# Kernel tuning notes

Measured on AMD Instinct MI355X. Metric: run time of the kernel, lower is better.

## Reference

```python
import jax, jax.numpy as jnp
import numpy as np

SIZES = [4096, 12288, 20480, 20480, 8192]  # atoms of degree 0..4 (atoms sorted by degree)
N_ATOMS = sum(SIZES)
BATCH = 1024
N_TASKS, N_CLASSES = 12, 2
BN_EPS = 1e-3  # keras BatchNormalization default epsilon


def setup_inputs() -> dict:
    key = jax.random.key(0)
    ks = jax.random.split(key, 20)
    inp = {}
    inp["atom_features"] = jax.random.normal(ks[0], (N_ATOMS, 75), jnp.float32)
    starts = np.concatenate([[0], np.cumsum(SIZES)[:-1]])
    inp["degree_slice"] = jnp.asarray(np.stack([starts, np.array(SIZES)], 1), jnp.int32)
    inp["membership"] = jax.random.randint(ks[1], (N_ATOMS,), 0, BATCH, jnp.int32)
    inp["n_samples"] = BATCH
    for d in range(1, 5):
        inp[f"deg_adj_{d}"] = jax.random.randint(ks[1 + d], (SIZES[d], d), 0, N_ATOMS, jnp.int32)

    def w(k, shape, s=0.05):
        return s * jax.random.normal(k, shape, jnp.float32)

    # GraphConv weights: order [relW_deg1, selfW_deg1, ..., relW_deg4, selfW_deg4, selfW_deg0]
    inp["gc1_W"] = w(ks[6], (9, 75, 256)); inp["gc1_b"] = w(ks[7], (9, 256))
    inp["gc2_W"] = w(ks[8], (9, 256, 256)); inp["gc2_b"] = w(ks[9], (9, 256))

    def bn_params(k, c):  # rows: gamma, beta, moving_mean, moving_var
        g = 1.0 + 0.1 * jax.random.normal(k, (c,), jnp.float32)
        b = 0.1 * jax.random.normal(jax.random.fold_in(k, 1), (c,), jnp.float32)
        return jnp.stack([g, b, jnp.zeros((c,), jnp.float32), jnp.ones((c,), jnp.float32)])

    inp["bn1"] = bn_params(ks[10], 256)
    inp["bn2"] = bn_params(ks[11], 256)
    inp["bn3"] = bn_params(ks[12], 512)
    inp["dense_W"] = w(ks[13], (256, 512)); inp["dense_b"] = w(ks[14], (512,))
    inp["head_W"] = w(ks[15], (2 * 512, N_TASKS * N_CLASSES)); inp["head_b"] = w(ks[16], (N_TASKS * N_CLASSES,))
    return inp


def _graph_conv(x, adjs, W, b):
    # degree-0 atoms: self transform only (last weight matrix)
    pieces = [x[: SIZES[0]] @ W[8] + b[8]]
    off = SIZES[0]
    for d in range(1, 5):
        nd = SIZES[d]
        self_atoms = x[off: off + nd]
        rel = jnp.take(x, adjs[d - 1], axis=0).sum(axis=1)  # [nd, F] neighbor sum
        out = rel @ W[2 * (d - 1)] + b[2 * (d - 1)] + self_atoms @ W[2 * d - 1] + b[2 * d - 1]
        pieces.append(out)
        off += nd
    return jax.nn.relu(jnp.concatenate(pieces, axis=0))


def _graph_pool(x, adjs):
    pieces = [x[: SIZES[0]]]  # degree-0: passthrough
    off = SIZES[0]
    for d in range(1, 5):
        nd = SIZES[d]
        self_atoms = x[off: off + nd]
        neigh = jnp.take(x, adjs[d - 1], axis=0)  # [nd, d, F]
        pieces.append(jnp.maximum(self_atoms, neigh.max(axis=1)))
        off += nd
    return jnp.concatenate(pieces, axis=0)


def _bn(x, p):  # inference batchnorm with moving stats
    g, b, m, v = p
    return g * (x - m) * jax.lax.rsqrt(v + BN_EPS) + b


def reference(atom_features, degree_slice, membership, n_samples,
              deg_adj_1, deg_adj_2, deg_adj_3, deg_adj_4,
              gc1_W, gc1_b, gc2_W, gc2_b, bn1, bn2, bn3,
              dense_W, dense_b, head_W, head_b):
    adjs = (deg_adj_1, deg_adj_2, deg_adj_3, deg_adj_4)
    x = atom_features
    for W, b, bn in ((gc1_W, gc1_b, bn1), (gc2_W, gc2_b, bn2)):
        x = _bn(_graph_conv(x, adjs, W, b), bn)
        x = _graph_pool(x, adjs)
    h = _bn(jax.nn.relu(x @ dense_W + dense_b), bn3)  # [N_ATOMS, 512]
    # GraphGather: per-molecule sum and max, tanh activation
    seg_sum = jax.ops.segment_sum(h, membership, num_segments=BATCH)
    seg_max = jax.ops.segment_max(h, membership, num_segments=BATCH)
    fp = jnp.tanh(jnp.concatenate([seg_sum, seg_max], axis=1))  # neural fingerprint [BATCH, 1024]
    logits = (fp @ head_W + head_b).reshape(BATCH, N_TASKS, N_CLASSES)[: int(n_samples)]  # trim
    return jax.nn.softmax(logits, axis=-1), logits, fp
```

## Files before the change

### kernel.cpp

```cpp
#include <hip/hip_runtime.h>
#include <hip/hip_bf16.h>
#include <math.h>

#define NA 65536
#define MAXSEG 160

typedef _Float16 half8 __attribute__((ext_vector_type(8)));
typedef _Float16 h4    __attribute__((ext_vector_type(4)));
typedef float float4v  __attribute__((ext_vector_type(4)));

typedef __attribute__((address_space(3))) unsigned int lds_uint;
typedef __attribute__((address_space(1))) const unsigned int g_uint;

__device__ __forceinline__ void async16(const void* g, void* l) {
    __builtin_amdgcn_global_load_lds((g_uint*)g, (lds_uint*)l, 16, 0, 0);
}


__device__ __forceinline__ int unperm128(int p) {
    return (p & ~127) + (((p & 127) & 7) << 4) + ((p & 127) >> 3);
}

__device__ __forceinline__ void atom_seg(int atom, int& d, int& loc,
                                         const int* a1, const int* a2,
                                         const int* a3, const int* a4,
                                         const int*& adj) {
    if (atom < 4096)       { d = 0; loc = 0; adj = nullptr; }
    else if (atom < 16384) { d = 1; adj = a1; loc = atom - 4096; }
    else if (atom < 36864) { d = 2; adj = a2; loc = atom - 16384; }
    else if (atom < 57344) { d = 3; adj = a3; loc = atom - 36864; }
    else                   { d = 4; adj = a4; loc = atom - 57344; }
}

__global__ __launch_bounds__(256) void prep_kernel(
    const float* __restrict__ af,
    const float* __restrict__ gc1W, const float* __restrict__ gc1b,
    const float* __restrict__ gc2W, const float* __restrict__ gc2b,
    const float* __restrict__ dW, const float* __restrict__ hW,
    _Float16* __restrict__ af16, _Float16* __restrict__ Wc1, float* __restrict__ bias1,
    _Float16* __restrict__ Wc2, float* __restrict__ bias2,
    _Float16* __restrict__ dWt, float* __restrict__ hWt, int* __restrict__ count) {
    int b = blockIdx.x, t = threadIdx.x;
    if (b < 5120) {
        int idx = b * 256 + t;
        int atom = idx / 20, k4 = idx - atom * 20;
        int c0 = k4 * 4;
        h4 o;
        #pragma unroll
        for (int j = 0; j < 4; j++) {
            int c = c0 + j;
            o[j] = (_Float16)((c < 75) ? af[(size_t)atom * 75 + c] : 0.f);
        }
        *(h4*)(af16 + (size_t)atom * 80 + c0) = o;
    } else if (b < 5920) {
        int idx = (b - 5120) * 256 + t;
        if (idx < 204800) {
            int k = idx % 160, n = (idx / 160) & 255, seg = idx / (160 * 256);
            float v = 0.f;
            if (k < 80) {
                if (k < 75) { int w = (seg == 0) ? 8 : (2 * seg - 1); v = gc1W[(w * 75 + k) * 256 + n]; }
            } else {
                int kk = k - 80;
                if (kk < 75 && seg > 0) { int w = 2 * (seg - 1); v = gc1W[(w * 75 + kk) * 256 + n]; }
            }
            Wc1[(size_t)(seg * 256 + n) * 160 + k] = (_Float16)v;
        }
        if (idx < 1280) {
            int n = idx & 255, seg = idx >> 8;
            bias1[idx] = (seg == 0) ? gc1b[8 * 256 + n]
                                    : gc1b[(2 * seg - 1) * 256 + n] + gc1b[2 * (seg - 1) * 256 + n];
        }
    } else if (b < 8480) {
        int idx = (b - 5920) * 256 + t;
        int k = idx & 511, n = (idx >> 9) & 255, seg = idx >> 17;
        float v = 0.f;
        if (k < 256) {
            int w = (seg == 0) ? 8 : (2 * seg - 1);
            v = gc2W[(w * 256 + unperm128(k)) * 256 + n];
        } else if (seg > 0) {
            int w = 2 * (seg - 1);
            v = gc2W[(w * 256 + unperm128(k - 256)) * 256 + n];
        }
        Wc2[(size_t)(seg * 256 + n) * 512 + k] = (_Float16)v;
        if (idx < 1280) {
            int nn = idx & 255, sg = idx >> 8;
            bias2[idx] = (sg == 0) ? gc2b[8 * 256 + nn]
                                   : gc2b[(2 * sg - 1) * 256 + nn] + gc2b[2 * (sg - 1) * 256 + nn];
        }
    } else if (b < 8992) {
        int idx = (b - 8480) * 256 + t;
        int n = idx >> 8, k = idx & 255;
        dWt[(size_t)n * 256 + k] = (_Float16)dW[(size_t)unperm128(k) * 512 + n];
    } else if (b < 9088) {
        int idx = (b - 8992) * 256 + t;
        int o = idx / 1024, k = idx & 1023;
        hWt[idx] = hW[k * 24 + o];
    } else {
        int i = (b - 9088) * 256 + t;
        if (i < 1024) count[i] = 0;
    }
}

__global__ void bucket_kernel(const int* __restrict__ mem, int* __restrict__ count,
                              int* __restrict__ list) {
    int i = blockIdx.x * 256 + threadIdx.x;
    int seg = mem[i];
    int pos = atomicAdd(&count[seg], 1);
    if (pos < MAXSEG) list[seg * MAXSEG + pos] = i;
}

__global__ __launch_bounds__(256) void gather1n_kernel(
    const _Float16* __restrict__ af16,
    const int* __restrict__ a1, const int* __restrict__ a2,
    const int* __restrict__ a3, const int* __restrict__ a4,
    _Float16* __restrict__ Xn1) {
    int idx = blockIdx.x * 256 + threadIdx.x;
    int atom = idx / 20, k4 = idx - atom * 20;
    int c0 = k4 * 4;
    int d, loc; const int* adj;
    atom_seg(atom, d, loc, a1, a2, a3, a4, adj);
    float s0 = 0.f, s1 = 0.f, s2 = 0.f, s3 = 0.f;
    for (int j = 0; j < d; j++) {
        int nb = adj[(size_t)loc * d + j];
        h4 v = *(const h4*)(af16 + (size_t)nb * 80 + c0);
        s0 += (float)v[0]; s1 += (float)v[1]; s2 += (float)v[2]; s3 += (float)v[3];
    }
    h4 o; o[0] = (_Float16)s0; o[1] = (_Float16)s1; o[2] = (_Float16)s2; o[3] = (_Float16)s3;
    *(h4*)(Xn1 + (size_t)atom * 80 + c0) = o;
}

__global__ __launch_bounds__(256) void gather2n_kernel(
    const _Float16* __restrict__ p,
    const int* __restrict__ a1, const int* __restrict__ a2,
    const int* __restrict__ a3, const int* __restrict__ a4,
    _Float16* __restrict__ Xn) {
    int atom = blockIdx.x * 8 + (threadIdx.x >> 5);
    int l = threadIdx.x & 31;
    int d, loc; const int* adj;
    atom_seg(atom, d, loc, a1, a2, a3, a4, adj);
    float s[8] = {};
    for (int j = 0; j < d; j++) {
        int nb = adj[(size_t)loc * d + j];
        half8 v = *(const half8*)(p + (size_t)nb * 256 + l * 8);
        #pragma unroll
        for (int e = 0; e < 8; e++) s[e] += (float)v[e];
    }
    half8 o;
    #pragma unroll
    for (int e = 0; e < 8; e++) o[e] = (_Float16)s[e];
    *(half8*)(Xn + (size_t)atom * 256 + l * 8) = o;
}

template<int K, int N, int BK, int SB>
__global__ __launch_bounds__(256) void gemm_kernel(
    const _Float16* __restrict__ X, const _Float16* __restrict__ Xn,
    const _Float16* __restrict__ Wt,
    const float* __restrict__ bias, const float* __restrict__ bnp,
    int wstride, int bstride, _Float16* __restrict__ out) {
    constexpr int NC8 = BK / 8;
    constexpr int MASK = NC8 - 1;
    __shared__ __align__(16) _Float16 As[128 * BK];
    __shared__ __align__(16) _Float16 Bs[128 * BK];
    constexpr int nb = N / 128;
    int G = gridDim.x;
    int bid = (blockIdx.x & 7) * (G >> 3) + (blockIdx.x >> 3);
    int m0 = (bid / nb) * 128, n0 = (bid % nb) * 128;
    int t = m0 >> 7;
    int seg = (t < 32) ? 0 : (t < 128) ? 1 : (t < 288) ? 2 : (t < 448) ? 3 : 4;
    const _Float16* Wb = Wt + (size_t)seg * wstride;
    const float* bia = bias + seg * bstride;
    int tid = threadIdx.x, lane = tid & 63, wave = tid >> 6;
    int wm = (wave >> 1) * 64, wn = (wave & 1) * 64;
    int lrow = lane & 15, lq = lane >> 4;
    float4v acc[4][4] = {};
    for (int kc = 0; kc < K / BK; kc++) {
        #pragma unroll
        for (int q = 0; q < NC8 / 2; q++) {
            int slot = q * 256 + wave * 64 + lane;
            int row = slot / NC8;
            int cs = slot & MASK;
            int c8 = cs ^ (row & MASK);
            const _Float16* gA;
            if (SB == 0) {
                gA = X + (size_t)(m0 + row) * K + kc * BK + c8 * 8;
            } else {
                int kcol = kc * BK + c8 * 8;
                gA = (kcol < SB) ? X  + (size_t)(m0 + row) * SB + kcol
                                 : Xn + (size_t)(m0 + row) * SB + (kcol - SB);
            }
            async16(gA, As + (size_t)(q * 256 + wave * 64) * 8);
            const _Float16* gB = Wb + (size_t)(n0 + row) * K + kc * BK + c8 * 8;
            async16(gB, Bs + (size_t)(q * 256 + wave * 64) * 8);
        }
        __syncthreads();
        #pragma unroll
        for (int kl = 0; kl < BK / 32; kl++) {
            half8 af[4], bf[4];
            #pragma unroll
            for (int i = 0; i < 4; i++) {
                int ra = wm + i * 16 + lrow;
                int ca = (kl * 4 + lq) ^ (ra & MASK);
                af[i] = *(const half8*)(As + ra * BK + ca * 8);
                int rb = wn + i * 16 + lrow;
                int cb = (kl * 4 + lq) ^ (rb & MASK);
                bf[i] = *(const half8*)(Bs + rb * BK + cb * 8);
            }
            #pragma unroll
            for (int mi = 0; mi < 4; mi++)
                #pragma unroll
                for (int ni = 0; ni < 4; ni++)
                    acc[mi][ni] = __builtin_amdgcn_mfma_f32_16x16x32_f16(af[mi], bf[ni], acc[mi][ni], 0, 0, 0);
        }
        __syncthreads();
    }
    float bv[4], sc[4], mn[4], be[4];
    #pragma unroll
    for (int ni = 0; ni < 4; ni++) {
        int c = n0 + wn + ni * 16 + lrow;
        bv[ni] = bia[c];
        float g = bnp[c], vr = bnp[3 * N + c];
        mn[ni] = bnp[2 * N + c]; be[ni] = bnp[N + c];
        sc[ni] = g * rsqrtf(vr + 1e-3f);
    }
    int p0 = n0 + lrow * 8 + (wave & 1) * 4;
    #pragma unroll
    for (int mi = 0; mi < 4; mi++) {
        #pragma unroll
        for (int r = 0; r < 4; r++) {
            h4 pack;
            #pragma unroll
            for (int ni = 0; ni < 4; ni++) {
                float v = acc[mi][ni][r] + bv[ni];
                v = fmaxf(v, 0.f);
                v = sc[ni] * (v - mn[ni]) + be[ni];
                pack[ni] = (_Float16)v;
            }
            int row = m0 + wm + mi * 16 + lq * 4 + r;
            *(h4*)(out + (size_t)row * N + p0) = pack;
        }
    }
}

__global__ __launch_bounds__(256) void pool_f16_kernel(
    const _Float16* __restrict__ x,
    const int* __restrict__ a1, const int* __restrict__ a2,
    const int* __restrict__ a3, const int* __restrict__ a4,
    _Float16* __restrict__ out) {
    int atom = blockIdx.x * 8 + (threadIdx.x >> 5);
    int l = threadIdx.x & 31;
    int d, loc; const int* adj;
    atom_seg(atom, d, loc, a1, a2, a3, a4, adj);
    half8 m = *(const half8*)(x + (size_t)atom * 256 + l * 8);
    float mv[8];
    #pragma unroll
    for (int e = 0; e < 8; e++) mv[e] = (float)m[e];
    for (int j = 0; j < d; j++) {
        int nb = adj[(size_t)loc * d + j];
        half8 v = *(const half8*)(x + (size_t)nb * 256 + l * 8);
        #pragma unroll
        for (int e = 0; e < 8; e++) mv[e] = fmaxf(mv[e], (float)v[e]);
    }
    half8 o;
    #pragma unroll
    for (int e = 0; e < 8; e++) o[e] = (_Float16)mv[e];
    *(half8*)(out + (size_t)atom * 256 + l * 8) = o;
}

__global__ __launch_bounds__(512) void seg_reduce_kernel(
    const _Float16* __restrict__ h, const int* __restrict__ count,
    const int* __restrict__ list, float* __restrict__ fp) {
    int seg = blockIdx.x, c = threadIdx.x;
    int chan = unperm128(c);
    int n = count[seg]; if (n > MAXSEG) n = MAXSEG;
    float sum = 0.f, mx = -INFINITY;
    for (int a = 0; a < n; a++) {
        int row = list[seg * MAXSEG + a];
        float v = (float)h[(size_t)row * 512 + c];
        sum += v; mx = fmaxf(mx, v);
    }
    fp[(size_t)seg * 1024 + chan] = tanhf(sum);
    fp[(size_t)seg * 1024 + 512 + chan] = tanhf(mx);
}

__global__ __launch_bounds__(256) void head_kernel(
    const float* __restrict__ fp, const float* __restrict__ hWt,
    const float* __restrict__ hb, float* __restrict__ logits,
    float* __restrict__ probs) {
    __shared__ float fps[1024];
    __shared__ float red[32];
    int s = blockIdx.x;
    for (int i = threadIdx.x; i < 1024; i += 256) fps[i] = fp[(size_t)s * 1024 + i];
    __syncthreads();
    int t = threadIdx.x;
    int o = t >> 3, kp = t & 7;
    float acc = 0.f;
    if (o < 24) {
        const float* w = hWt + (size_t)o * 1024 + kp * 128;
        const float* f = fps + kp * 128;
        #pragma unroll 8
        for (int i = 0; i < 128; i++) acc = fmaf(f[i], w[i], acc);
    }
    acc += __shfl_down(acc, 4, 64);
    acc += __shfl_down(acc, 2, 64);
    acc += __shfl_down(acc, 1, 64);
    if (o < 24 && kp == 0) red[o] = acc + hb[o];
    __syncthreads();
    if (t < 24) {
        float a = red[t];
        float an = red[t ^ 1];
        logits[(size_t)s * 24 + t] = a;
        probs[(size_t)s * 24 + t] = 1.f / (1.f + expf(an - a));
    }
}

extern "C" void kernel_launch(void* const* d_in, const int* in_sizes, int n_in,
                              void* d_out, int out_size, void* d_ws, size_t ws_size,
                              hipStream_t stream) {
    const float* af         = (const float*)d_in[0];
    const int*   membership = (const int*)d_in[2];
    const int*   a1 = (const int*)d_in[4];
    const int*   a2 = (const int*)d_in[5];
    const int*   a3 = (const int*)d_in[6];
    const int*   a4 = (const int*)d_in[7];
    const float* gc1W = (const float*)d_in[8];
    const float* gc1b = (const float*)d_in[9];
    const float* gc2W = (const float*)d_in[10];
    const float* gc2b = (const float*)d_in[11];
    const float* bn1  = (const float*)d_in[12];
    const float* bn2  = (const float*)d_in[13];
    const float* bn3  = (const float*)d_in[14];
    const float* dW   = (const float*)d_in[15];
    const float* db   = (const float*)d_in[16];
    const float* hW   = (const float*)d_in[17];
    const float* hb   = (const float*)d_in[18];

    float* out    = (float*)d_out;
    float* probs  = out;
    float* logits = out + 24576;
    float* fp     = out + 49152;

    _Float16* Wc1  = (_Float16*)d_ws;
    _Float16* Wc2  = Wc1 + 204800;
    _Float16* dWt  = Wc2 + 655360;
    float* bias1   = (float*)(dWt + 131072);
    float* bias2   = bias1 + 1280;
    float* hWt     = bias2 + 1280;
    int* count     = (int*)(hWt + 24576);
    int* list      = count + 1024;
    _Float16* bufBig = (_Float16*)(list + 163840);
    _Float16* bufY   = bufBig + (size_t)NA * 512;
    _Float16* bufP   = bufY + (size_t)NA * 256;
    _Float16* af16 = bufBig;
    _Float16* Xn1  = bufBig + (size_t)NA * 80;
    _Float16* Xn   = bufBig + (size_t)NA * 256;
    _Float16* h    = bufBig;

    prep_kernel<<<9092, 256, 0, stream>>>(af, gc1W, gc1b, gc2W, gc2b, dW, hW,
                                          af16, Wc1, bias1, Wc2, bias2, dWt, hWt, count);
    bucket_kernel<<<256, 256, 0, stream>>>(membership, count, list);
    gather1n_kernel<<<5120, 256, 0, stream>>>(af16, a1, a2, a3, a4, Xn1);
    gemm_kernel<160, 256, 32, 80><<<1024, 256, 0, stream>>>(af16, Xn1, Wc1, bias1, bn1,
                                                            256 * 160, 256, bufY);
    pool_f16_kernel<<<8192, 256, 0, stream>>>(bufY, a1, a2, a3, a4, bufP);
    gather2n_kernel<<<8192, 256, 0, stream>>>(bufP, a1, a2, a3, a4, Xn);
    gemm_kernel<512, 256, 64, 256><<<1024, 256, 0, stream>>>(bufP, Xn, Wc2, bias2, bn2,
                                                             256 * 512, 256, bufY);
    pool_f16_kernel<<<8192, 256, 0, stream>>>(bufY, a1, a2, a3, a4, bufP);
    gemm_kernel<256, 512, 64, 0><<<2048, 256, 0, stream>>>(bufP, nullptr, dWt, db, bn3,
                                                           0, 0, h);
    seg_reduce_kernel<<<1024, 512, 0, stream>>>(h, count, list, fp);
    head_kernel<<<1024, 256, 0, stream>>>(fp, hWt, hb, logits, probs);
}
```

Before: 311.8 us.

## Fuse neighbor gather into GEMM2 and segment reduction into dense GEMM epilogue

The separate gather2n kernel is removed. The second graph-conv GEMM now computes neighbor sums on the fly while staging its A tile, and uses a 128x256 tile so each row block runs in a single pass. The dense layer now reads atoms in membership-sorted order, built by new scan and sort kernels. Its epilogue reduces sum and max per molecule in LDS bins, then flushes them with global atomics, which removes the 64MB h write and the seg_reduce pass. The costs are a serialized gather inside the GEMM main loop, float atomics that make the sum order nondeterministic, and added small kernels for sorting.

```diff
diff --git a/kernel.cpp b/kernel.cpp
--- a/kernel.cpp
+++ b/kernel.cpp
@@ -20,6 +20,12 @@
 __device__ __forceinline__ int unperm128(int p) {
     return (p & ~127) + (((p & 127) & 7) << 4) + ((p & 127) >> 3);
 }
+
+__device__ __forceinline__ unsigned mapf(float x) {
+    unsigned b = __float_as_uint(x);
+    return (b & 0x80000000u) ? ~b : (b | 0x80000000u);
+}
+#define MAPF_NEGINF 0x007FFFFFu
 
 __device__ __forceinline__ void atom_seg(int atom, int& d, int& loc,
                                          const int* a1, const int* a2,
@@ -39,7 +45,8 @@
     const float* __restrict__ dW, const float* __restrict__ hW,
     _Float16* __restrict__ af16, _Float16* __restrict__ Wc1, float* __restrict__ bias1,
     _Float16* __restrict__ Wc2, float* __restrict__ bias2,
-    _Float16* __restrict__ dWt, float* __restrict__ hWt, int* __restrict__ count) {
+    _Float16* __restrict__ dWt, float* __restrict__ hWt, int* __restrict__ count,
+    float* __restrict__ fpsum, unsigned* __restrict__ fpmaxu) {
     int b = blockIdx.x, t = threadIdx.x;
     if (b < 5120) {
         int idx = b * 256 + t;
@@ -95,9 +102,13 @@
         int idx = (b - 8992) * 256 + t;
         int o = idx / 1024, k = idx & 1023;
         hWt[idx] = hW[k * 24 + o];
-    } else {
+    } else if (b < 9092) {
         int i = (b - 9088) * 256 + t;
         if (i < 1024) count[i] = 0;
+    } else if (b < 11140) {
+        fpsum[(size_t)(b - 9092) * 256 + t] = 0.f;
+    } else {
+        fpmaxu[(size_t)(b - 11140) * 256 + t] = MAPF_NEGINF;
     }
 }
 
@@ -107,6 +118,32 @@
     int seg = mem[i];
     int pos = atomicAdd(&count[seg], 1);
     if (pos < MAXSEG) list[seg * MAXSEG + pos] = i;
+}
+
+__global__ __launch_bounds__(1024) void scan_kernel(const int* __restrict__ count,
+                                                    int* __restrict__ offs) {
+    __shared__ int tmp[1024];
+    int t = threadIdx.x;
+    int v = count[t]; if (v > MAXSEG) v = MAXSEG;
+    tmp[t] = v;
+    __syncthreads();
+    for (int off = 1; off < 1024; off <<= 1) {
+        int x = (t >= off) ? tmp[t - off] : 0;
+        __syncthreads();
+        tmp[t] += x;
+        __syncthreads();
+    }
+    offs[t] = tmp[t] - v;
+}
+
+__global__ __launch_bounds__(256) void build_sorted_kernel(
+    const int* __restrict__ count, const int* __restrict__ offs,
+    const int* __restrict__ list, int* __restrict__ sorted) {
+    int seg = blockIdx.x;
+    int n = count[seg]; if (n > MAXSEG) n = MAXSEG;
+    int base = offs[seg];
+    for (int i = threadIdx.x; i < n; i += 256)
+        sorted[base + i] = list[seg * MAXSEG + i] | (seg << 16);
 }
 
 __global__ __launch_bounds__(256) void gather1n_kernel(
@@ -127,28 +164,6 @@
     }
     h4 o; o[0] = (_Float16)s0; o[1] = (_Float16)s1; o[2] = (_Float16)s2; o[3] = (_Float16)s3;
     *(h4*)(Xn1 + (size_t)atom * 80 + c0) = o;
-}
-
-__global__ __launch_bounds__(256) void gather2n_kernel(
-    const _Float16* __restrict__ p,
-    const int* __restrict__ a1, const int* __restrict__ a2,
-    const int* __restrict__ a3, const int* __restrict__ a4,
-    _Float16* __restrict__ Xn) {
-    int atom = blockIdx.x * 8 + (threadIdx.x >> 5);
-    int l = threadIdx.x & 31;
-    int d, loc; const int* adj;
-    atom_seg(atom, d, loc, a1, a2, a3, a4, adj);
-    float s[8] = {};
-    for (int j = 0; j < d; j++) {
-        int nb = adj[(size_t)loc * d + j];
-        half8 v = *(const half8*)(p + (size_t)nb * 256 + l * 8);
-        #pragma unroll
-        for (int e = 0; e < 8; e++) s[e] += (float)v[e];
-    }
-    half8 o;
-    #pragma unroll
-    for (int e = 0; e < 8; e++) o[e] = (_Float16)s[e];
-    *(half8*)(Xn + (size_t)atom * 256 + l * 8) = o;
 }
 
 template<int K, int N, int BK, int SB>
@@ -241,6 +256,116 @@
     }
 }
 
+__global__ __launch_bounds__(256, 2) void gemm2_kernel(
+    const _Float16* __restrict__ p, const _Float16* __restrict__ Wt,
+    const float* __restrict__ bias, const float* __restrict__ bnp,
+    const int* __restrict__ a1, const int* __restrict__ a2,
+    const int* __restrict__ a3, const int* __restrict__ a4,
+    _Float16* __restrict__ out) {
+    __shared__ __align__(16) _Float16 As[128 * 64];
+    __shared__ __align__(16) _Float16 Bs[256 * 64];
+    int G = gridDim.x;
+    int bid = (blockIdx.x & 7) * (G >> 3) + (blockIdx.x >> 3);
+    int m0 = bid * 128;
+    int t8 = m0 >> 7;
+    int seg = (t8 < 32) ? 0 : (t8 < 128) ? 1 : (t8 < 288) ? 2 : (t8 < 448) ? 3 : 4;
+    int segstart = (seg == 0) ? 0 : (seg == 1) ? 4096 : (seg == 2) ? 16384 : (seg == 3) ? 36864 : 57344;
+    const int* adj = (seg == 1) ? a1 : (seg == 2) ? a2 : (seg == 3) ? a3 : (seg == 4) ? a4 : nullptr;
+    int d = seg;
+    int loc0 = m0 - segstart;
+    const _Float16* Wb = Wt + (size_t)seg * 256 * 512;
+    const float* bia = bias + seg * 256;
+    int tid = threadIdx.x, lane = tid & 63, wave = tid >> 6;
+    int wm = (wave >> 1) * 64, wn = (wave & 1) * 128;
+    int lrow = lane & 15, lq = lane >> 4;
+    float4v acc[4][8] = {};
+    for (int kc = 0; kc < 8; kc++) {
+        if (kc < 4) {
+            #pragma unroll
+            for (int q = 0; q < 4; q++) {
+                int slot = q * 256 + wave * 64 + lane;
+                int row = slot >> 3, cs = slot & 7, c8 = cs ^ (row & 7);
+                async16(p + (size_t)(m0 + row) * 256 + kc * 64 + c8 * 8,
+                        As + (size_t)(q * 256 + wave * 64) * 8);
+            }
+        } else {
+            #pragma unroll
+            for (int q = 0; q < 4; q++) {
+                int slot = q * 256 + wave * 64 + lane;
+                int row = slot >> 3, cs = slot & 7, c8 = cs ^ (row & 7);
+                int col = (kc - 4) * 64 + c8 * 8;
+                float s[8] = {};
+                for (int j = 0; j < d; j++) {
+                    int nb = adj[(size_t)(loc0 + row) * d + j];
+                    half8 v = *(const half8*)(p + (size_t)nb * 256 + col);
+                    #pragma unroll
+                    for (int e = 0; e < 8; e++) s[e] += (float)v[e];
+                }
+                half8 o;
+                #pragma unroll
+                for (int e = 0; e < 8; e++) o[e] = (_Float16)s[e];
+                *(half8*)(As + row * 64 + cs * 8) = o;
+            }
+        }
+        #pragma unroll
+        for (int q = 0; q < 8; q++) {
+            int slot = q * 256 + wave * 64 + lane;
+            int row = slot >> 3, cs = slot & 7, c8 = cs ^ (row & 7);
+            async16(Wb + (size_t)row * 512 + kc * 64 + c8 * 8,
+                    Bs + (size_t)(q * 256 + wave * 64) * 8);
+        }
+        __syncthreads();
+        #pragma unroll
+        for (int kl = 0; kl < 2; kl++) {
+            half8 af[4], bf[8];
+            #pragma unroll
+            for (int i = 0; i < 4; i++) {
+                int ra = wm + i * 16 + lrow;
+                int ca = (kl * 4 + lq) ^ (ra & 7);
+                af[i] = *(const half8*)(As + ra * 64 + ca * 8);
+            }
+            #pragma unroll
+            for (int j = 0; j < 8; j++) {
+                int rb = wn + j * 16 + lrow;
+                int cb = (kl * 4 + lq) ^ (rb & 7);
+                bf[j] = *(const half8*)(Bs + rb * 64 + cb * 8);
+            }
+            #pragma unroll
+            for (int mi = 0; mi < 4; mi++)
+                #pragma unroll
+                for (int ni = 0; ni < 8; ni++)
+                    acc[mi][ni] = __builtin_amdgcn_mfma_f32_16x16x32_f16(af[mi], bf[ni], acc[mi][ni], 0, 0, 0);
+        }
+        __syncthreads();
+    }
+    float bv[8], sc[8], mn[8], be[8];
+    #pragma unroll
+    for (int ni = 0; ni < 8; ni++) {
+        int c = wn + ni * 16 + lrow;
+        bv[ni] = bia[c];
+        float g = bnp[c], vr = bnp[3 * 256 + c];
+        mn[ni] = bnp[2 * 256 + c]; be[ni] = bnp[256 + c];
+        sc[ni] = g * rsqrtf(vr + 1e-3f);
+    }
+    int p0 = wn + lrow * 8;
+    #pragma unroll
+    for (int mi = 0; mi < 4; mi++) {
+        #pragma unroll
+        for (int r = 0; r < 4; r++) {
+            half8 pack;
+            #pragma unroll
+            for (int ni = 0; ni < 8; ni++) {
+                float v = acc[mi][ni][r] + bv[ni];
+                v = fmaxf(v, 0.f);
+                v = sc[ni] * (v - mn[ni]) + be[ni];
+                pack[ni] = (_Float16)v;
+            }
+            int row = m0 + wm + mi * 16 + lq * 4 + r;
+            *(half8*)(out + (size_t)row * 256 + p0) = pack;
+        }
+    }
+}
+
 __global__ __launch_bounds__(256) void pool_f16_kernel(
     const _Float16* __restrict__ x,
     const int* __restrict__ a1, const int* __restrict__ a2,
@@ -266,30 +391,142 @@
     *(half8*)(out + (size_t)atom * 256 + l * 8) = o;
 }
 
-__global__ __launch_bounds__(512) void seg_reduce_kernel(
-    const _Float16* __restrict__ h, const int* __restrict__ count,
-    const int* __restrict__ list, float* __restrict__ fp) {
-    int seg = blockIdx.x, c = threadIdx.x;
-    int chan = unperm128(c);
-    int n = count[seg]; if (n > MAXSEG) n = MAXSEG;
-    float sum = 0.f, mx = -INFINITY;
-    for (int a = 0; a < n; a++) {
-        int row = list[seg * MAXSEG + a];
-        float v = (float)h[(size_t)row * 512 + c];
-        sum += v; mx = fmaxf(mx, v);
-    }
-    fp[(size_t)seg * 1024 + chan] = tanhf(sum);
-    fp[(size_t)seg * 1024 + 512 + chan] = tanhf(mx);
+__global__ __launch_bounds__(256) void dense_kernel(
+    const _Float16* __restrict__ X, const _Float16* __restrict__ Wt,
+    const float* __restrict__ bias, const float* __restrict__ bnp,
+    const int* __restrict__ sorted,
+    float* __restrict__ fpsum, unsigned* __restrict__ fpmaxu) {
+    constexpr int NBINS = 32;
+    __shared__ __align__(16) _Float16 As[128 * 64];
+    __shared__ __align__(16) _Float16 Bs[128 * 64];
+    __shared__ float binsum[NBINS * 128];
+    __shared__ unsigned binmax[NBINS * 128];
+    __shared__ int spk[128];
+    int G = gridDim.x;
+    int bid = (blockIdx.x & 7) * (G >> 3) + (blockIdx.x >> 3);
+    int m0 = (bid >> 2) * 128, n0 = (bid & 3) * 128;
+    int tid = threadIdx.x, lane = tid & 63, wave = tid >> 6;
+    if (tid < 128) spk[tid] = sorted[m0 + tid];
+    for (int e = tid; e < NBINS * 128; e += 256) { binsum[e] = 0.f; binmax[e] = MAPF_NEGINF; }
+    __syncthreads();
+    const _Float16* baseA[4]; const _Float16* baseB[4];
+    #pragma unroll
+    for (int q = 0; q < 4; q++) {
+        int slot = q * 256 + wave * 64 + lane;
+        int row = slot >> 3, cs = slot & 7, c8 = cs ^ (row & 7);
+        baseA[q] = X + (size_t)(spk[row] & 0xFFFF) * 256 + c8 * 8;
+        baseB[q] = Wt + (size_t)(n0 + row) * 256 + c8 * 8;
+    }
+    int wm = (wave >> 1) * 64, wn = (wave & 1) * 64;
+    int lrow = lane & 15, lq = lane >> 4;
+    float4v acc[4][4] = {};
+    for (int kc = 0; kc < 4; kc++) {
+        #pragma unroll
+        for (int q = 0; q < 4; q++) {
+            async16(baseA[q] + kc * 64, As + (size_t)(q * 256 + wave * 64) * 8);
+            async16(baseB[q] + kc * 64, Bs + (size_t)(q * 256 + wave * 64) * 8);
+        }
+        __syncthreads();
+        #pragma unroll
+        for (int kl = 0; kl < 2; kl++) {
+            half8 af[4], bf[4];
+            #pragma unroll
+            for (int i = 0; i < 4; i++) {
+                int ra = wm + i * 16 + lrow;
+                int ca = (kl * 4 + lq) ^ (ra & 7);
+                af[i] = *(const half8*)(As + ra * 64 + ca * 8);
+                int rb = wn + i * 16 + lrow;
+                int cb = (kl * 4 + lq) ^ (rb & 7);
+                bf[i] = *(const half8*)(Bs + rb * 64 + cb * 8);
+            }
+            #pragma unroll
+            for (int mi = 0; mi < 4; mi++)
+                #pragma unroll
+                for (int ni = 0; ni < 4; ni++)
+                    acc[mi][ni] = __builtin_amdgcn_mfma_f32_16x16x32_f16(af[mi], bf[ni], acc[mi][ni], 0, 0, 0);
+        }
+        __syncthreads();
+    }
+    float bv[4], sc[4], mn[4], be[4];
+    #pragma unroll
+    for (int ni = 0; ni < 4; ni++) {
+        int c = n0 + wn + ni * 16 + lrow;
+        bv[ni] = bias[c];
+        float g = bnp[c], vr = bnp[3 * 512 + c];
+        mn[ni] = bnp[2 * 512 + c]; be[ni] = bnp[512 + c];
+        sc[ni] = g * rsqrtf(vr + 1e-3f);
+    }
+    int pcol = lrow * 8 + (wave & 1) * 4;
+    int segbase = spk[0] >> 16;
+    int curs = -1;
+    float ps[4], pm[4];
+    #pragma unroll
+    for (int mi = 0; mi < 4; mi++) {
+        #pragma unroll
+        for (int r = 0; r < 4; r++) {
+            int row = wm + mi * 16 + lq * 4 + r;
+            int srel = (spk[row] >> 16) - segbase;
+            if (srel > NBINS - 1) srel = NBINS - 1;
+            if (srel != curs) {
+                if (curs >= 0) {
+                    int bb = curs * 128 + pcol;
+                    #pragma unroll
+                    for (int ni = 0; ni < 4; ni++) {
+                        atomicAdd(&binsum[bb + ni], ps[ni]);
+                        atomicMax(&binmax[bb + ni], mapf(pm[ni]));
+                    }
+                }
+                curs = srel;
+                #pragma unroll
+                for (int ni = 0; ni < 4; ni++) { ps[ni] = 0.f; pm[ni] = -INFINITY; }
+            }
+            #pragma unroll
+            for (int ni = 0; ni < 4; ni++) {
+                float v = acc[mi][ni][r] + bv[ni];
+                v = fmaxf(v, 0.f);
+                v = sc[ni] * (v - mn[ni]) + be[ni];
+                ps[ni] += v;
+                pm[ni] = fmaxf(pm[ni], v);
+            }
+        }
+    }
+    {
+        int bb = curs * 128 + pcol;
+        #pragma unroll
+        for (int ni = 0; ni < 4; ni++) {
+            atomicAdd(&binsum[bb + ni], ps[ni]);
+            atomicMax(&binmax[bb + ni], mapf(pm[ni]));
+        }
+    }
+    __syncthreads();
+    int nseg = (spk[127] >> 16) - segbase + 1;
+    if (nseg > NBINS) nseg = NBINS;
+    for (int e = tid; e < nseg * 128; e += 256) {
+        int s = e >> 7, pc = e & 127;
+        float v = binsum[e];
+        if (v != 0.f) atomicAdd(&fpsum[(size_t)(segbase + s) * 512 + n0 + pc], v);
+        unsigned u = binmax[e];
+        if (u != MAPF_NEGINF) atomicMax(&fpmaxu[(size_t)(segbase + s) * 512 + n0 + pc], u);
+    }
 }
 
 __global__ __launch_bounds__(256) void head_kernel(
-    const float* __restrict__ fp, const float* __restrict__ hWt,
-    const float* __restrict__ hb, float* __restrict__ logits,
-    float* __restrict__ probs) {
+    const float* __restrict__ fpsum, const unsigned* __restrict__ fpmaxu,
+    const float* __restrict__ hWt, const float* __restrict__ hb,
+    float* __restrict__ fp, float* __restrict__ logits, float* __restrict__ probs) {
     __shared__ float fps[1024];
     __shared__ float red[32];
     int s = blockIdx.x;
-    for (int i = threadIdx.x; i < 1024; i += 256) fps[i] = fp[(size_t)s * 1024 + i];
+    for (int i = threadIdx.x; i < 512; i += 256) {
+        float sv = tanhf(fpsum[(size_t)s * 512 + i]);
+        unsigned u = fpmaxu[(size_t)s * 512 + i];
+        unsigned b = (u & 0x80000000u) ? (u & 0x7FFFFFFFu) : ~u;
+        float mv = tanhf(__uint_as_float(b));
+        int chan = unperm128(i);
+        fps[chan] = sv; fps[512 + chan] = mv;
+        fp[(size_t)s * 1024 + chan] = sv;
+        fp[(size_t)s * 1024 + 512 + chan] = mv;
+    }
     __syncthreads();
     int t = threadIdx.x;
     int o = t >> 3, kp = t & 7;
@@ -345,29 +582,30 @@
     float* bias1   = (float*)(dWt + 131072);
     float* bias2   = bias1 + 1280;
     float* hWt     = bias2 + 1280;
-    int* count     = (int*)(hWt + 24576);
-    int* list      = count + 1024;
-    _Float16* bufBig = (_Float16*)(list + 163840);
-    _Float16* bufY   = bufBig + (size_t)NA * 512;
+    float* fpsum   = hWt + 24576;
+    unsigned* fpmaxu = (unsigned*)(fpsum + 524288);
+    int* count     = (int*)(fpmaxu + 524288);
+    int* offs      = count + 1024;
+    int* sorted    = offs + 1024;
+    int* list      = sorted + 65536;
+    _Float16* bufSm  = (_Float16*)(list + 163840);
+    _Float16* bufY   = bufSm + (size_t)NA * 160;
     _Float16* bufP   = bufY + (size_t)NA * 256;
-    _Float16* af16 = bufBig;
-    _Float16* Xn1  = bufBig + (size_t)NA * 80;
-    _Float16* Xn   = bufBig + (size_t)NA * 256;
-    _Float16* h    = bufBig;
-
-    prep_kernel<<<9092, 256, 0, stream>>>(af, gc1W, gc1b, gc2W, gc2b, dW, hW,
-                                          af16, Wc1, bias1, Wc2, bias2, dWt, hWt, count);
+    _Float16* af16 = bufSm;
+    _Float16* Xn1  = bufSm + (size_t)NA * 80;
+
+    prep_kernel<<<13188, 256, 0, stream>>>(af, gc1W, gc1b, gc2W, gc2b, dW, hW,
+                                           af16, Wc1, bias1, Wc2, bias2, dWt, hWt,
+                                           count, fpsum, fpmaxu);
     bucket_kernel<<<256, 256, 0, stream>>>(membership, count, list);
+    scan_kernel<<<1, 1024, 0, stream>>>(count, offs);
+    build_sorted_kernel<<<1024, 256, 0, stream>>>(count, offs, list, sorted);
     gather1n_kernel<<<5120, 256, 0, stream>>>(af16, a1, a2, a3, a4, Xn1);
     gemm_kernel<160, 256, 32, 80><<<1024, 256, 0, stream>>>(af16, Xn1, Wc1, bias1, bn1,
                                                             256 * 160, 256, bufY);
     pool_f16_kernel<<<8192, 256, 0, stream>>>(bufY, a1, a2, a3, a4, bufP);
-    gather2n_kernel<<<8192, 256, 0, stream>>>(bufP, a1, a2, a3, a4, Xn);
-    gemm_kernel<512, 256, 64, 256><<<1024, 256, 0, stream>>>(bufP, Xn, Wc2, bias2, bn2,
-                                                             256 * 512, 256, bufY);
+    gemm2_kernel<<<512, 256, 0, stream>>>(bufP, Wc2, bias2, bn2, a1, a2, a3, a4, bufY);
     pool_f16_kernel<<<8192, 256, 0, stream>>>(bufY, a1, a2, a3, a4, bufP);
-    gemm_kernel<256, 512, 64, 0><<<2048, 256, 0, stream>>>(bufP, nullptr, dWt, db, bn3,
-                                                           0, 0, h);
-    seg_reduce_kernel<<<1024, 512, 0, stream>>>(h, count, list, fp);
-    head_kernel<<<1024, 256, 0, stream>>>(fp, hWt, hb, logits, probs);
-}
+    dense_kernel<<<2048, 256, 0, stream>>>(bufP, dWt, db, bn3, sorted, fpsum, fpmaxu);
+    head_kernel<<<1024, 256, 0, stream>>>(fpsum, fpmaxu, hWt, hb, fp, logits, probs);
+}
```

Result: slower. 321.8 us (+3.2%).
